# Optimization experiments

Hardware: AMD Instinct MI355X
Metric: run time of the kernel (lower is better)

## Reference

```python
import jax, jax.numpy as jnp
import numpy as np

N_SRC = 50000
N_EDGES = 150000
D_IN = 512
D_OUT = 512

def setup_inputs() -> dict:
    key = jax.random.key(0)
    k1, k2, k3, k4, k5 = jax.random.split(key, 5)
    src_h = jax.random.normal(k1, (N_SRC, D_IN), dtype=jnp.float32)
    W = jax.random.normal(k2, (D_OUT, D_IN), dtype=jnp.float32) * (1.0 / np.sqrt(D_IN))
    b = jax.random.normal(k3, (D_OUT,), dtype=jnp.float32) * 0.01
    src_idx = jax.random.randint(k4, (N_EDGES,), 0, N_SRC, dtype=jnp.int64) if jax.config.jax_enable_x64 else jax.random.randint(k4, (N_EDGES,), 0, N_SRC, dtype=jnp.int32)
    dst_idx = jax.random.randint(k5, (N_EDGES,), 0, N_SRC, dtype=src_idx.dtype)
    return {"src_h": src_h, "W": W, "b": b, "src_idx": src_idx, "dst_idx": dst_idx, "n_dst": N_SRC}

def reference(src_h, W, b, src_idx, dst_idx, n_dst):
    # message passing: copy src feature to each edge, sum into dst nodes
    msgs = src_h[src_idx]                                  # [E, D_in]
    agg = jax.ops.segment_sum(msgs, dst_idx, num_segments=n_dst)  # [N_dst, D_in]
    # dense linear (apply_linear == 'linear' -> no relu)
    return agg @ W.T + b                                   # [N_dst, D_out]
```

## Files before the change

### kernel.cpp

```cpp
#include <hip/hip_runtime.h>
#include <hip/hip_bf16.h>

#define D 512
#define BM 128
#define BN 128
#define BK 32
#define SB 512

typedef __attribute__((ext_vector_type(8))) short bf16x8;
typedef __attribute__((ext_vector_type(4))) float f32x4;

__device__ __forceinline__ unsigned short bf16_rne(float f) {
    union { float f; unsigned u; } v; v.f = f;
    return (unsigned short)((v.u + 0x7FFFu + ((v.u >> 16) & 1u)) >> 16);
}

__device__ __forceinline__ void gload16(const void* g, void* l) {
    __builtin_amdgcn_global_load_lds(
        (const __attribute__((address_space(1))) void*)g,
        (__attribute__((address_space(3))) void*)l,
        16, 0, 0);
}

__device__ __forceinline__ void facc(float4& a, const float4 v) {
    a.x += v.x; a.y += v.y; a.z += v.z; a.w += v.w;
}

__global__ __launch_bounds__(256) void prep_kernel(const float* __restrict__ W,
                                                   unsigned short* __restrict__ wb,
                                                   const int* __restrict__ dst, int E,
                                                   int* __restrict__ cnt) {
    const int b = blockIdx.x;
    const int t = threadIdx.x;
    if (b < 512) {
        const int i = b * 256 + t;
        float2 v = ((const float2*)W)[i];
        unsigned r = ((unsigned)bf16_rne(v.x)) | (((unsigned)bf16_rne(v.y)) << 16);
        ((unsigned*)wb)[i] = r;
    } else {
        const int e = (b - 512) * 256 + t;
        if (e < E) atomicAdd(&cnt[dst[e]], 1);
    }
}


__global__ __launch_bounds__(256) void scan_reduce_kernel(const int* __restrict__ cnt, int M,
                                                          int* __restrict__ bsum) {
    const int t = threadIdx.x;
    const int i0 = blockIdx.x * SB + t * 2;
    int v = 0;
    if (i0 < M)     v += cnt[i0];
    if (i0 + 1 < M) v += cnt[i0 + 1];
    #pragma unroll
    for (int o = 32; o > 0; o >>= 1) v += __shfl_down(v, o, 64);
    __shared__ int ws_[4];
    if ((t & 63) == 0) ws_[t >> 6] = v;
    __syncthreads();
    if (t == 0) bsum[blockIdx.x] = ws_[0] + ws_[1] + ws_[2] + ws_[3];
}

__global__ __launch_bounds__(256) void scan_bsum_kernel(const int* __restrict__ bsum, int NB,
                                                        int* __restrict__ bscan,
                                                        int* __restrict__ offsets, int M) {
    __shared__ int s[256];
    const int t = threadIdx.x;
    int v = (t < NB) ? bsum[t] : 0;
    s[t] = v;
    __syncthreads();
    #pragma unroll
    for (int o = 1; o < 256; o <<= 1) {
        int u = (t >= o) ? s[t - o] : 0;
        __syncthreads();
        s[t] += u;
        __syncthreads();
    }
    if (t < NB) bscan[t] = s[t] - v;
    if (t == 255) offsets[M] = s[255];
}

__global__ __launch_bounds__(256) void scan_final_kernel(int* __restrict__ cnt, int M,
                                                         const int* __restrict__ bscan,
                                                         int* __restrict__ offsets) {
    __shared__ int s[256];
    const int t = threadIdx.x;
    const int base = blockIdx.x * SB + t * 2;
    int a = (base < M) ? cnt[base] : 0;
    int b = (base + 1 < M) ? cnt[base + 1] : 0;
    const int tsum = a + b;
    s[t] = tsum;
    __syncthreads();
    #pragma unroll
    for (int o = 1; o < 256; o <<= 1) {
        int u = (t >= o) ? s[t - o] : 0;
        __syncthreads();
        s[t] += u;
        __syncthreads();
    }
    const int excl = s[t] - tsum + bscan[blockIdx.x];
    if (base < M)     { offsets[base] = excl;         cnt[base] = excl; }
    if (base + 1 < M) { offsets[base + 1] = excl + a; cnt[base + 1] = excl + a; }
}

__global__ __launch_bounds__(256) void sort_kernel(const int* __restrict__ src,
                                                   const int* __restrict__ dst, int E,
                                                   int* __restrict__ cursor,
                                                   int* __restrict__ sorted_src) {
    int e = blockIdx.x * 256 + threadIdx.x;
    if (e < E) {
        int pos = atomicAdd(&cursor[dst[e]], 1);
        sorted_src[pos] = src[e];
    }
}

__global__ __launch_bounds__(256) void agg_kernel(const float* __restrict__ src_h,
                                                  const int* __restrict__ offsets,
                                                  const int* __restrict__ sorted_src,
                                                  unsigned short* __restrict__ aggb,
                                                  int M) {
    const int wv = threadIdx.x >> 6;
    const int lane = threadIdx.x & 63;
    const int d = blockIdx.x * 4 + wv;
    if (d >= M) return;
    const int beg = offsets[d];
    const int end = offsets[d + 1];
    const float4* rb = (const float4*)src_h;

    float4 a0 = {0.f, 0.f, 0.f, 0.f};
    float4 a1 = {0.f, 0.f, 0.f, 0.f};
    int e = beg;

    for (; e + 4 <= end; e += 4) {
        const int s0 = sorted_src[e];
        const int s1 = sorted_src[e + 1];
        const int s2 = sorted_src[e + 2];
        const int s3 = sorted_src[e + 3];
        float4 v00 = rb[(size_t)s0 * 128 + lane];
        float4 v01 = rb[(size_t)s0 * 128 + 64 + lane];
        float4 v10 = rb[(size_t)s1 * 128 + lane];
        float4 v11 = rb[(size_t)s1 * 128 + 64 + lane];
        float4 v20 = rb[(size_t)s2 * 128 + lane];
        float4 v21 = rb[(size_t)s2 * 128 + 64 + lane];
        float4 v30 = rb[(size_t)s3 * 128 + lane];
        float4 v31 = rb[(size_t)s3 * 128 + 64 + lane];
        facc(a0, v00); facc(a1, v01);
        facc(a0, v10); facc(a1, v11);
        facc(a0, v20); facc(a1, v21);
        facc(a0, v30); facc(a1, v31);
    }
    if (e + 2 <= end) {
        const int s0 = sorted_src[e];
        const int s1 = sorted_src[e + 1];
        float4 v00 = rb[(size_t)s0 * 128 + lane];
        float4 v01 = rb[(size_t)s0 * 128 + 64 + lane];
        float4 v10 = rb[(size_t)s1 * 128 + lane];
        float4 v11 = rb[(size_t)s1 * 128 + 64 + lane];
        facc(a0, v00); facc(a1, v01);
        facc(a0, v10); facc(a1, v11);
        e += 2;
    }
    if (e < end) {
        const int s0 = sorted_src[e];
        float4 v00 = rb[(size_t)s0 * 128 + lane];
        float4 v01 = rb[(size_t)s0 * 128 + 64 + lane];
        facc(a0, v00); facc(a1, v01);
    }

    ushort4 o0, o1;
    o0.x = bf16_rne(a0.x); o0.y = bf16_rne(a0.y);
    o0.z = bf16_rne(a0.z); o0.w = bf16_rne(a0.w);
    o1.x = bf16_rne(a1.x); o1.y = bf16_rne(a1.y);
    o1.z = bf16_rne(a1.z); o1.w = bf16_rne(a1.w);
    *(ushort4*)(aggb + (size_t)d * D + lane * 4) = o0;
    *(ushort4*)(aggb + (size_t)d * D + 256 + lane * 4) = o1;
}


__global__ __launch_bounds__(256) void gemm_kernel(const unsigned short* __restrict__ A,
                                                   const unsigned short* __restrict__ B,
                                                   const float* __restrict__ bias,
                                                   float* __restrict__ out,
                                                   int M, int MB_tiles) {
    __shared__ __align__(16) unsigned short As[BM * BK];
    __shared__ __align__(16) unsigned short Bs[BN * BK];

    const int L = blockIdx.x;
    const int mb = (L >> 5) * 8 + (L & 7);
    const int nb = (L >> 3) & 3;
    if (mb >= MB_tiles) return;
    const int m0 = mb * BM;
    const int n0 = nb * BN;

    const int t = threadIdx.x;
    const int lane = t & 63;
    const int wave = t >> 6;
    const int wm = wave >> 1;
    const int wn = wave & 1;
    const int quad = lane >> 4;
    const int lr = lane & 15;

    const int srow = t >> 2;
    const int scol = ((t & 3) ^ ((t >> 3) & 3)) * 8;
    const int arow0 = min(m0 + srow, M - 1);
    const int arow1 = min(m0 + 64 + srow, M - 1);
    const int brow0 = n0 + srow;
    const int brow1 = n0 + 64 + srow;

    const int fsw = (quad ^ ((lr >> 1) & 3)) * 8;

    f32x4 acc[4][4] = {};

    for (int k0 = 0; k0 < D; k0 += BK) {
        gload16(A + (size_t)arow0 * D + k0 + scol, As + t * 8);
        gload16(A + (size_t)arow1 * D + k0 + scol, As + 2048 + t * 8);
        gload16(B + (size_t)brow0 * D + k0 + scol, Bs + t * 8);
        gload16(B + (size_t)brow1 * D + k0 + scol, Bs + 2048 + t * 8);
        __syncthreads();

        bf16x8 af[4], bfr[4];
        #pragma unroll
        for (int i = 0; i < 4; ++i) {
            af[i]  = *(const bf16x8*)&As[(wm * 64 + i * 16 + lr) * BK + fsw];
            bfr[i] = *(const bf16x8*)&Bs[(wn * 64 + i * 16 + lr) * BK + fsw];
        }
        #pragma unroll
        for (int i = 0; i < 4; ++i)
            #pragma unroll
            for (int j = 0; j < 4; ++j)
                acc[i][j] = __builtin_amdgcn_mfma_f32_16x16x32_bf16(af[i], bfr[j], acc[i][j], 0, 0, 0);
        __syncthreads();
    }

    #pragma unroll
    for (int j = 0; j < 4; ++j) {
        const int col = n0 + wn * 64 + j * 16 + lr;
        const float bv = bias[col];
        #pragma unroll
        for (int i = 0; i < 4; ++i) {
            const int rbase = m0 + wm * 64 + i * 16 + quad * 4;
            #pragma unroll
            for (int r = 0; r < 4; ++r) {
                const int row = rbase + r;
                if (row < M) out[(size_t)row * D + col] = acc[i][j][r] + bv;
            }
        }
    }
}

extern "C" void kernel_launch(void* const* d_in, const int* in_sizes, int n_in,
                              void* d_out, int out_size, void* d_ws, size_t ws_size,
                              hipStream_t stream) {
    const float* src_h = (const float*)d_in[0];
    const float* W     = (const float*)d_in[1];
    const float* b     = (const float*)d_in[2];
    const int*   si    = (const int*)d_in[3];
    const int*   di    = (const int*)d_in[4];
    const int M = in_sizes[0] / D;
    const int E = in_sizes[3];
    const int NB = (M + SB - 1) / SB;

    char* ws = (char*)d_ws;
    unsigned short* aggb = (unsigned short*)ws;
    unsigned short* wb   = (unsigned short*)(ws + 51200000);
    int* offsets         = (int*)(ws + 51724288);
    int* cnt             = (int*)(ws + 51924480);
    int* ssrc            = (int*)(ws + 52124480);
    int* bsum            = (int*)(ws + 52724480);
    int* bscan           = (int*)(ws + 52726480);

    hipMemsetAsync(cnt, 0, (size_t)M * sizeof(int), stream);
    const int HB = (E + 255) / 256;
    prep_kernel<<<dim3(512 + HB), 256, 0, stream>>>(W, wb, di, E, cnt);
    scan_reduce_kernel<<<dim3(NB), 256, 0, stream>>>(cnt, M, bsum);
    scan_bsum_kernel<<<1, 256, 0, stream>>>(bsum, NB, bscan, offsets, M);
    scan_final_kernel<<<dim3(NB), 256, 0, stream>>>(cnt, M, bscan, offsets);
    sort_kernel<<<dim3((E + 255) / 256), 256, 0, stream>>>(si, di, E, cnt, ssrc);
    agg_kernel<<<dim3((M + 3) / 4), 256, 0, stream>>>(src_h, offsets, ssrc, aggb, M);

    const int MB_tiles = (M + BM - 1) / BM;
    const int ngrid = ((MB_tiles + 7) / 8) * 32;
    gemm_kernel<<<dim3(ngrid), 256, 0, stream>>>(aggb, wb, b, (float*)d_out, M, MB_tiles);
}
```

Measured before the change: 310.0 us.

## Fuse gather-aggregation into GEMM, keeping aggregated tile in LDS

Merges the aggregation and GEMM kernels into one. Each 512-thread block gathers and sums 64 destination rows into a swizzled bf16 LDS tile covering the full K=512. Each of its 8 waves then computes a 64x64 output slice, reading W fragments directly from global memory. This removes the 51MB bf16 intermediate write and read-back and one kernel launch. The cost is B fragments loaded from global/L2 without LDS staging, a 64KB LDS tile that limits occupancy, and GEMM work serialized behind the gather within each block.

Result: slower. 325.1 us (+4.9%).

```diff
diff --git a/kernel.cpp b/kernel.cpp
--- a/kernel.cpp
+++ b/kernel.cpp
@@ -2,10 +2,8 @@
 #include <hip/hip_bf16.h>
 
 #define D 512
-#define BM 128
-#define BN 128
-#define BK 32
 #define SB 512
+#define FBM 64
 
 typedef __attribute__((ext_vector_type(8))) short bf16x8;
 typedef __attribute__((ext_vector_type(4))) float f32x4;
@@ -13,13 +11,6 @@
 __device__ __forceinline__ unsigned short bf16_rne(float f) {
     union { float f; unsigned u; } v; v.f = f;
     return (unsigned short)((v.u + 0x7FFFu + ((v.u >> 16) & 1u)) >> 16);
-}
-
-__device__ __forceinline__ void gload16(const void* g, void* l) {
-    __builtin_amdgcn_global_load_lds(
-        (const __attribute__((address_space(1))) void*)g,
-        (__attribute__((address_space(3))) void*)l,
-        16, 0, 0);
 }
 
 __device__ __forceinline__ void facc(float4& a, const float4 v) {
@@ -112,131 +103,107 @@
     }
 }
 
-__global__ __launch_bounds__(256) void agg_kernel(const float* __restrict__ src_h,
-                                                  const int* __restrict__ offsets,
-                                                  const int* __restrict__ sorted_src,
-                                                  unsigned short* __restrict__ aggb,
-                                                  int M) {
-    const int wv = threadIdx.x >> 6;
-    const int lane = threadIdx.x & 63;
-    const int d = blockIdx.x * 4 + wv;
-    if (d >= M) return;
-    const int beg = offsets[d];
-    const int end = offsets[d + 1];
+__global__ __launch_bounds__(512, 2) void fused_kernel(const float* __restrict__ src_h,
+                                                       const int* __restrict__ offsets,
+                                                       const int* __restrict__ sorted_src,
+                                                       const unsigned short* __restrict__ wb,
+                                                       const float* __restrict__ bias,
+                                                       float* __restrict__ out, int M) {
+    __shared__ __align__(16) unsigned short As[FBM * D];
+
+    const int t = threadIdx.x;
+    const int w = t >> 6;
+    const int lane = t & 63;
+    const int m0 = blockIdx.x * FBM;
     const float4* rb = (const float4*)src_h;
 
-    float4 a0 = {0.f, 0.f, 0.f, 0.f};
-    float4 a1 = {0.f, 0.f, 0.f, 0.f};
-    int e = beg;
-
-    for (; e + 4 <= end; e += 4) {
-        const int s0 = sorted_src[e];
-        const int s1 = sorted_src[e + 1];
-        const int s2 = sorted_src[e + 2];
-        const int s3 = sorted_src[e + 3];
-        float4 v00 = rb[(size_t)s0 * 128 + lane];
-        float4 v01 = rb[(size_t)s0 * 128 + 64 + lane];
-        float4 v10 = rb[(size_t)s1 * 128 + lane];
-        float4 v11 = rb[(size_t)s1 * 128 + 64 + lane];
-        float4 v20 = rb[(size_t)s2 * 128 + lane];
-        float4 v21 = rb[(size_t)s2 * 128 + 64 + lane];
-        float4 v30 = rb[(size_t)s3 * 128 + lane];
-        float4 v31 = rb[(size_t)s3 * 128 + 64 + lane];
-        facc(a0, v00); facc(a1, v01);
-        facc(a0, v10); facc(a1, v11);
-        facc(a0, v20); facc(a1, v21);
-        facc(a0, v30); facc(a1, v31);
-    }
-    if (e + 2 <= end) {
-        const int s0 = sorted_src[e];
-        const int s1 = sorted_src[e + 1];
-        float4 v00 = rb[(size_t)s0 * 128 + lane];
-        float4 v01 = rb[(size_t)s0 * 128 + 64 + lane];
-        float4 v10 = rb[(size_t)s1 * 128 + lane];
-        float4 v11 = rb[(size_t)s1 * 128 + 64 + lane];
-        facc(a0, v00); facc(a1, v01);
-        facc(a0, v10); facc(a1, v11);
-        e += 2;
-    }
-    if (e < end) {
-        const int s0 = sorted_src[e];
-        float4 v00 = rb[(size_t)s0 * 128 + lane];
-        float4 v01 = rb[(size_t)s0 * 128 + 64 + lane];
-        facc(a0, v00); facc(a1, v01);
-    }
-
-    ushort4 o0, o1;
-    o0.x = bf16_rne(a0.x); o0.y = bf16_rne(a0.y);
-    o0.z = bf16_rne(a0.z); o0.w = bf16_rne(a0.w);
-    o1.x = bf16_rne(a1.x); o1.y = bf16_rne(a1.y);
-    o1.z = bf16_rne(a1.z); o1.w = bf16_rne(a1.w);
-    *(ushort4*)(aggb + (size_t)d * D + lane * 4) = o0;
-    *(ushort4*)(aggb + (size_t)d * D + 256 + lane * 4) = o1;
-}
-
-
-__global__ __launch_bounds__(256) void gemm_kernel(const unsigned short* __restrict__ A,
-                                                   const unsigned short* __restrict__ B,
-                                                   const float* __restrict__ bias,
-                                                   float* __restrict__ out,
-                                                   int M, int MB_tiles) {
-    __shared__ __align__(16) unsigned short As[BM * BK];
-    __shared__ __align__(16) unsigned short Bs[BN * BK];
-
-    const int L = blockIdx.x;
-    const int mb = (L >> 5) * 8 + (L & 7);
-    const int nb = (L >> 3) & 3;
-    if (mb >= MB_tiles) return;
-    const int m0 = mb * BM;
-    const int n0 = nb * BN;
-
-    const int t = threadIdx.x;
-    const int lane = t & 63;
-    const int wave = t >> 6;
-    const int wm = wave >> 1;
-    const int wn = wave & 1;
+    for (int rr = 0; rr < 8; ++rr) {
+        const int r = w * 8 + rr;
+        const int rg = m0 + r;
+        int beg = 0, end = 0;
+        if (rg < M) { beg = offsets[rg]; end = offsets[rg + 1]; }
+        float4 a0 = {0.f, 0.f, 0.f, 0.f};
+        float4 a1 = {0.f, 0.f, 0.f, 0.f};
+        int e = beg;
+        for (; e + 4 <= end; e += 4) {
+            const int s0 = sorted_src[e];
+            const int s1 = sorted_src[e + 1];
+            const int s2 = sorted_src[e + 2];
+            const int s3 = sorted_src[e + 3];
+            float4 v00 = rb[(size_t)s0 * 128 + lane * 2];
+            float4 v01 = rb[(size_t)s0 * 128 + lane * 2 + 1];
+            float4 v10 = rb[(size_t)s1 * 128 + lane * 2];
+            float4 v11 = rb[(size_t)s1 * 128 + lane * 2 + 1];
+            float4 v20 = rb[(size_t)s2 * 128 + lane * 2];
+            float4 v21 = rb[(size_t)s2 * 128 + lane * 2 + 1];
+            float4 v30 = rb[(size_t)s3 * 128 + lane * 2];
+            float4 v31 = rb[(size_t)s3 * 128 + lane * 2 + 1];
+            facc(a0, v00); facc(a1, v01);
+            facc(a0, v10); facc(a1, v11);
+            facc(a0, v20); facc(a1, v21);
+            facc(a0, v30); facc(a1, v31);
+        }
+        if (e + 2 <= end) {
+            const int s0 = sorted_src[e];
+            const int s1 = sorted_src[e + 1];
+            float4 v00 = rb[(size_t)s0 * 128 + lane * 2];
+            float4 v01 = rb[(size_t)s0 * 128 + lane * 2 + 1];
+            float4 v10 = rb[(size_t)s1 * 128 + lane * 2];
+            float4 v11 = rb[(size_t)s1 * 128 + lane * 2 + 1];
+            facc(a0, v00); facc(a1, v01);
+            facc(a0, v10); facc(a1, v11);
+            e += 2;
+        }
+        if (e < end) {
+            const int s0 = sorted_src[e];
+            float4 v00 = rb[(size_t)s0 * 128 + lane * 2];
+            float4 v01 = rb[(size_t)s0 * 128 + lane * 2 + 1];
+            facc(a0, v00); facc(a1, v01);
+        }
+        union { bf16x8 v; unsigned short u[8]; } pk;
+        pk.u[0] = bf16_rne(a0.x); pk.u[1] = bf16_rne(a0.y);
+        pk.u[2] = bf16_rne(a0.z); pk.u[3] = bf16_rne(a0.w);
+        pk.u[4] = bf16_rne(a1.x); pk.u[5] = bf16_rne(a1.y);
+        pk.u[6] = bf16_rne(a1.z); pk.u[7] = bf16_rne(a1.w);
+        const int slot = lane ^ rr;
+        *(bf16x8*)&As[r * D + slot * 8] = pk.v;
+    }
+    __syncthreads();
+
     const int quad = lane >> 4;
     const int lr = lane & 15;
-
-    const int srow = t >> 2;
-    const int scol = ((t & 3) ^ ((t >> 3) & 3)) * 8;
-    const int arow0 = min(m0 + srow, M - 1);
-    const int arow1 = min(m0 + 64 + srow, M - 1);
-    const int brow0 = n0 + srow;
-    const int brow1 = n0 + 64 + srow;
-
-    const int fsw = (quad ^ ((lr >> 1) & 3)) * 8;
-
     f32x4 acc[4][4] = {};
 
-    for (int k0 = 0; k0 < D; k0 += BK) {
-        gload16(A + (size_t)arow0 * D + k0 + scol, As + t * 8);
-        gload16(A + (size_t)arow1 * D + k0 + scol, As + 2048 + t * 8);
-        gload16(B + (size_t)brow0 * D + k0 + scol, Bs + t * 8);
-        gload16(B + (size_t)brow1 * D + k0 + scol, Bs + 2048 + t * 8);
-        __syncthreads();
-
+    const unsigned short* wc0 = wb + (size_t)(w * 64 +  0 + lr) * D;
+    const unsigned short* wc1 = wb + (size_t)(w * 64 + 16 + lr) * D;
+    const unsigned short* wc2 = wb + (size_t)(w * 64 + 32 + lr) * D;
+    const unsigned short* wc3 = wb + (size_t)(w * 64 + 48 + lr) * D;
+
+    #pragma unroll 2
+    for (int k0 = 0; k0 < D; k0 += 32) {
         bf16x8 af[4], bfr[4];
+        const int ks = (k0 >> 3) + quad;
         #pragma unroll
-        for (int i = 0; i < 4; ++i) {
-            af[i]  = *(const bf16x8*)&As[(wm * 64 + i * 16 + lr) * BK + fsw];
-            bfr[i] = *(const bf16x8*)&Bs[(wn * 64 + i * 16 + lr) * BK + fsw];
-        }
+        for (int i = 0; i < 4; ++i)
+            af[i] = *(const bf16x8*)&As[(i * 16 + lr) * D + (ks ^ (lr & 7)) * 8];
+        bfr[0] = *(const bf16x8*)(wc0 + k0 + quad * 8);
+        bfr[1] = *(const bf16x8*)(wc1 + k0 + quad * 8);
+        bfr[2] = *(const bf16x8*)(wc2 + k0 + quad * 8);
+        bfr[3] = *(const bf16x8*)(wc3 + k0 + quad * 8);
         #pragma unroll
         for (int i = 0; i < 4; ++i)
             #pragma unroll
             for (int j = 0; j < 4; ++j)
                 acc[i][j] = __builtin_amdgcn_mfma_f32_16x16x32_bf16(af[i], bfr[j], acc[i][j], 0, 0, 0);
-        __syncthreads();
     }
 
     #pragma unroll
     for (int j = 0; j < 4; ++j) {
-        const int col = n0 + wn * 64 + j * 16 + lr;
+        const int col = w * 64 + j * 16 + lr;
         const float bv = bias[col];
         #pragma unroll
         for (int i = 0; i < 4; ++i) {
-            const int rbase = m0 + wm * 64 + i * 16 + quad * 4;
+            const int rbase = m0 + i * 16 + quad * 4;
             #pragma unroll
             for (int r = 0; r < 4; ++r) {
                 const int row = rbase + r;
@@ -259,7 +226,6 @@
     const int NB = (M + SB - 1) / SB;
 
     char* ws = (char*)d_ws;
-    unsigned short* aggb = (unsigned short*)ws;
     unsigned short* wb   = (unsigned short*)(ws + 51200000);
     int* offsets         = (int*)(ws + 51724288);
     int* cnt             = (int*)(ws + 51924480);
@@ -274,9 +240,8 @@
     scan_bsum_kernel<<<1, 256, 0, stream>>>(bsum, NB, bscan, offsets, M);
     scan_final_kernel<<<dim3(NB), 256, 0, stream>>>(cnt, M, bscan, offsets);
     sort_kernel<<<dim3((E + 255) / 256), 256, 0, stream>>>(si, di, E, cnt, ssrc);
-    agg_kernel<<<dim3((M + 3) / 4), 256, 0, stream>>>(src_h, offsets, ssrc, aggb, M);
-
-    const int MB_tiles = (M + BM - 1) / BM;
-    const int ngrid = ((MB_tiles + 7) / 8) * 32;
-    gemm_kernel<<<dim3(ngrid), 256, 0, stream>>>(aggb, wb, b, (float*)d_out, M, MB_tiles);
-}
+
+    const int FB = (M + FBM - 1) / FBM;
+    fused_kernel<<<dim3(FB), 512, 0, stream>>>(src_h, offsets, ssrc, wb, b,
+                                               (float*)d_out, M);
+}
```
